# Kernel tuning notes

Hardware: AMD Instinct MI355X
Metric: run time of the kernel (lower is better)

## Reference

```python
import jax, jax.numpy as jnp
import numpy as np

N = 4096          # num_nodes
F = 64            # node_features
H = 128           # hidden_dim
NH = 4            # num_heads
HD = H // NH      # per-head dim = 32
L = 3             # num_layers
C = 7             # num_classes
EDGE_P = 0.004    # ~16 avg degree


def setup_inputs() -> dict:
    key = jax.random.key(0)
    ks = jax.random.split(key, 20)
    g = lambda k, shape, fan_in: jax.random.normal(k, shape, jnp.float32) / np.sqrt(fan_in)
    x = jax.random.normal(ks[0], (N, F), jnp.float32)
    adj = (jax.random.uniform(ks[1], (N, N)) < EDGE_P).astype(jnp.float32)
    return {
        "x": x,
        "adj": adj,
        "enc_W": g(ks[2], (F, H), F), "enc_b": jnp.zeros((H,), jnp.float32),
        "gcn_W": g(ks[3], (L, H, H), H), "gcn_b": jnp.zeros((L, H), jnp.float32),
        "attn_W": g(ks[4], (L, NH, H, HD), H), "attn_Wb": jnp.zeros((L, NH, HD), jnp.float32),
        "attn_a": g(ks[5], (L, NH, 2 * HD), 2 * HD), "attn_ab": jnp.zeros((L, NH), jnp.float32),
        "cls_W1": g(ks[6], (H, H // 2), H), "cls_b1": jnp.zeros((H // 2,), jnp.float32),
        "cls_W2": g(ks[7], (H // 2, C), H // 2), "cls_b2": jnp.zeros((C,), jnp.float32),
        "con_W1": g(ks[8], (H, H // 2), H), "con_b1": jnp.zeros((H // 2,), jnp.float32),
        "con_W2": g(ks[9], (H // 2, 1), H // 2), "con_b2": jnp.zeros((1,), jnp.float32),
    }


def _normalize_adj(adj):
    a = adj + jnp.eye(adj.shape[0], dtype=adj.dtype)
    dinv = jnp.sum(a, axis=1) ** -0.5
    return dinv[:, None] * a * dinv[None, :]


def _gcn(h, adj_norm, W, b):
    support = adj_norm @ h                      # [N,H]
    return jax.nn.relu(support @ W + b)         # dropout=0 (eval)


def _attention(h, edge_mask, W, Wb, a, ab):
    # h:[N,H], W:[NH,H,HD], a:[NH,2*HD]; per-pair score = Linear(concat(h_i,h_j))
    hh = jnp.einsum('nf,hfd->hnd', h, W) + Wb[:, None, :]     # [NH,N,HD]
    a_src, a_dst = a[:, :HD], a[:, HD:]
    s_src = jnp.einsum('hnd,hd->hn', hh, a_src)               # [NH,N]
    s_dst = jnp.einsum('hnd,hd->hn', hh, a_dst)               # [NH,N]
    scores = s_src[:, :, None] + s_dst[:, None, :] + ab[:, None, None]
    # original uses literal 0.0 (NOT -inf) for non-edges before softmax
    scores = jnp.where(edge_mask[None, :, :], scores, 0.0)    # [NH,N,N]
    probs = jax.nn.softmax(scores, axis=-1)
    out = jnp.einsum('hij,hjd->hid', probs, hh)               # [NH,N,HD]
    return out.transpose(1, 0, 2).reshape(h.shape[0], NH * HD)


def reference(x, adj, enc_W, enc_b, gcn_W, gcn_b, attn_W, attn_Wb, attn_a, attn_ab,
              cls_W1, cls_b1, cls_W2, cls_b2, con_W1, con_b1, con_W2, con_b2):
    h = jax.nn.relu(x @ enc_W + enc_b)          # node encoder (dropout=0)
    adj_norm = _normalize_adj(adj)
    edge_mask = adj > 0
    for i in range(L):
        h_gcn = _gcn(h, adj_norm, gcn_W[i], gcn_b[i])
        h_attn = _attention(h, edge_mask, attn_W[i], attn_Wb[i], attn_a[i], attn_ab[i])
        h = jax.nn.relu(h_gcn + h_attn)
    node_logits = jax.nn.relu(h @ cls_W1 + cls_b1) @ cls_W2 + cls_b2
    h_mean = jnp.mean(h, axis=0, keepdims=True)
    contagion = jax.nn.relu(h_mean @ con_W1 + con_b1) @ con_W2 + con_b2
    return (node_logits, h, contagion)
```

## Files before the change

kernel.cpp:

```cpp
#include <hip/hip_runtime.h>

typedef unsigned short u16;
typedef unsigned int u32;

#define N 4096
#define F 64
#define H 128
#define NH 4
#define HD 32
#define EMAX 64

__device__ float g_hA[N * H];
__device__ float g_hB[N * H];
__device__ float g_hhA[N * H];
__device__ float g_hhB[N * H];
__device__ u16   g_cols[N * EMAX];
__device__ int   g_deg[N];
__device__ float g_dinv[N];
__device__ float g_ssrcA[N * NH];
__device__ float g_ssrcB[N * NH];
__device__ float g_sdstA[N * NH];
__device__ float g_sdstB[N * NH];
__device__ float g_part[3][32][H];
__device__ float g_hpart[32][H];

__global__ void k_csr(const float* __restrict__ adj) {
  __shared__ int cnt;
  int row = blockIdx.x;
  if (threadIdx.x == 0) cnt = 0;
  if (row == 0) {
    float* pz = &g_part[0][0][0];
    for (int i = threadIdx.x; i < 3 * 32 * H; i += 256) pz[i] = 0.f;
    float* hz = &g_hpart[0][0];
    for (int i = threadIdx.x; i < 32 * H; i += 256) hz[i] = 0.f;
  }
  __syncthreads();
  int base = threadIdx.x * 16;
  const float4* p = reinterpret_cast<const float4*>(adj + (size_t)row * N + base);
  float4 q0 = p[0], q1 = p[1], q2 = p[2], q3 = p[3];
  float vals[16] = {q0.x, q0.y, q0.z, q0.w, q1.x, q1.y, q1.z, q1.w,
                    q2.x, q2.y, q2.z, q2.w, q3.x, q3.y, q3.z, q3.w};
#pragma unroll
  for (int t = 0; t < 16; ++t)
    if (vals[t] != 0.f) {
      int pos = atomicAdd(&cnt, 1);
      if (pos < EMAX) g_cols[row * EMAX + pos] = (u16)(base + t);
    }
  __syncthreads();
  if (threadIdx.x == 0) {
    g_deg[row] = cnt < EMAX ? cnt : EMAX;
    g_dinv[row] = 1.0f / sqrtf((float)(cnt + 1));
  }
}

__device__ __forceinline__ void agg4(int i0, int tid, const float* __restrict__ h,
                                     const float* __restrict__ hhin,
                                     const float* __restrict__ ssrc_in,
                                     const float* __restrict__ sdst_in,
                                     int l, const float* __restrict__ abv,
                                     int (&jl)[4][EMAX], float (&dv)[4][EMAX],
                                     float (&sdl)[4][EMAX * NH],
                                     float& outa0, float& outa1,
                                     float& sup0, float& sup1) {
  int c = tid & 127, rg = tid >> 7, hc = c >> 5;
  int darr[4];
#pragma unroll
  for (int r = 0; r < 4; ++r) darr[r] = g_deg[i0 + r];
#pragma unroll
  for (int r = 0; r < 4; ++r) {
    const u16* cl = g_cols + (size_t)(i0 + r) * EMAX;
    for (int e = tid; e < darr[r]; e += 256) {
      int j = cl[e];
      jl[r][e] = j;
      dv[r][e] = g_dinv[j];
    }
  }
  __syncthreads();
#pragma unroll
  for (int r = 0; r < 4; ++r)
    for (int idx = tid; idx < darr[r] * NH; idx += 256)
      sdl[r][idx] = sdst_in[jl[r][idx >> 2] * NH + (idx & 3)];
  __syncthreads();

  float sumc = 0.f;
  const float* part = &g_part[l][0][0];
#pragma unroll
  for (int s = 0; s < 32; ++s) sumc += part[s * H + c];
  float ab = abv[hc];

  float oa[2], sp[2];
#pragma unroll
  for (int rr = 0; rr < 2; ++rr) {
    int r = rg * 2 + rr;
    int i = i0 + r, dd = darr[r];
    float ssrc = ssrc_in[i * NH + hc];
    float M = -INFINITY;
    for (int e = 0; e < dd; ++e) M = fmaxf(M, sdl[r][e * NH + hc]);
    float mv = fmaxf(0.f, ssrc + ab + M);
    float em = expf(-mv);
    float base = ssrc + ab - mv;
    float aA = 0.f, aT = 0.f, aG = 0.f, S = 0.f;
    int e = 0;
    for (; e + 2 <= dd; e += 2) {
      int j0 = jl[r][e], j1 = jl[r][e + 1];
      float q0 = hhin[j0 * H + c], q1 = hhin[j1 * H + c];
      float p0 = h[j0 * H + c], p1 = h[j1 * H + c];
      float w0 = expf(base + sdl[r][e * NH + hc]);
      float w1 = expf(base + sdl[r][(e + 1) * NH + hc]);
      aA = fmaf(w0, q0, aA); aA = fmaf(w1, q1, aA);
      aT += q0 + q1;
      aG = fmaf(dv[r][e], p0, aG); aG = fmaf(dv[r][e + 1], p1, aG);
      S += w0 + w1;
    }
    for (; e < dd; ++e) {
      int j = jl[r][e];
      float w = expf(base + sdl[r][e * NH + hc]);
      float q = hhin[j * H + c];
      aA = fmaf(w, q, aA);
      aT += q;
      aG = fmaf(dv[r][e], h[j * H + c], aG);
      S += w;
    }
    float Z = S + em * (float)(N - dd);
    oa[rr] = (aA + em * (sumc - aT)) / Z;
    float di = g_dinv[i];
    sp[rr] = di * (aG + di * h[i * H + c]);
  }
  outa0 = oa[0]; outa1 = oa[1]; sup0 = sp[0]; sup1 = sp[1];
}

__device__ __forceinline__ void proj4(int i0, int tid, const float (&hrowT)[H][4],
                                      const float* __restrict__ aW,
                                      const float* __restrict__ aWb,
                                      const float* __restrict__ aa, int lp,
                                      float* __restrict__ hhout,
                                      float* __restrict__ ssrc_out,
                                      float* __restrict__ sdst_out) {
  int c = tid & 127, rg = tid >> 7, hc = c >> 5, dc = c & 31;
  float b = aWb[hc * HD + dc];
  float p0 = b, p1 = b;
  for (int f = 0; f < H; ++f) {
    float w = aW[(hc * H + f) * HD + dc];
    float2 hv = *reinterpret_cast<const float2*>(&hrowT[f][rg * 2]);
    p0 = fmaf(hv.x, w, p0);
    p1 = fmaf(hv.y, w, p1);
  }
  int r0 = i0 + rg * 2, r1 = r0 + 1;
  hhout[r0 * H + c] = p0;
  hhout[r1 * H + c] = p1;
  const float* ap = aa + hc * 2 * HD;
  float as = ap[dc], ad = ap[HD + dc];
  float ss0 = p0 * as, ss1 = p1 * as, sd0 = p0 * ad, sd1 = p1 * ad;
#pragma unroll
  for (int m = 16; m >= 1; m >>= 1) {
    ss0 += __shfl_xor(ss0, m, 64); ss1 += __shfl_xor(ss1, m, 64);
    sd0 += __shfl_xor(sd0, m, 64); sd1 += __shfl_xor(sd1, m, 64);
  }
  if (dc == 0) {
    ssrc_out[r0 * NH + hc] = ss0; ssrc_out[r1 * NH + hc] = ss1;
    sdst_out[r0 * NH + hc] = sd0; sdst_out[r1 * NH + hc] = sd1;
  }
  atomicAdd(&g_part[lp][r0 & 31][c], p0);
  atomicAdd(&g_part[lp][r1 & 31][c], p1);
}

__global__ void k_enc_proj(const float* __restrict__ x, const float* __restrict__ eW,
                           const float* __restrict__ eb, const float* __restrict__ aW,
                           const float* __restrict__ aWb, const float* __restrict__ aa) {
  __shared__ float xT[F][4];
  __shared__ float hrowT[H][4];
  int i0 = blockIdx.x * 4, tid = threadIdx.x;
  int c = tid & 127, rg = tid >> 7;
  {
    int r = tid >> 6, k = tid & 63;
    xT[k][r] = x[(i0 + r) * F + k];
  }
  __syncthreads();
  float b = eb[c];
  float e0 = b, e1 = b;
  for (int k = 0; k < F; ++k) {
    float w = eW[k * H + c];
    float2 xv = *reinterpret_cast<const float2*>(&xT[k][rg * 2]);
    e0 = fmaf(xv.x, w, e0);
    e1 = fmaf(xv.y, w, e1);
  }
  e0 = fmaxf(e0, 0.f); e1 = fmaxf(e1, 0.f);
  int r0 = i0 + rg * 2, r1 = r0 + 1;
  g_hA[r0 * H + c] = e0; g_hA[r1 * H + c] = e1;
  hrowT[c][rg * 2] = e0; hrowT[c][rg * 2 + 1] = e1;
  __syncthreads();
  proj4(i0, tid, hrowT, aW, aWb, aa, 0, g_hhA, g_ssrcA, g_sdstA);
}

__global__ void k_acp(int pp, int l, const float* __restrict__ gW,
                      const float* __restrict__ gb, const float* __restrict__ aW,
                      const float* __restrict__ aWb, const float* __restrict__ aa,
                      const float* __restrict__ abv) {
  const float* h    = pp ? g_hB : g_hA;
  float*       hout = pp ? g_hA : g_hB;
  const float* hhin = pp ? g_hhB : g_hhA;
  float*       hhout= pp ? g_hhA : g_hhB;
  const float* ssin = pp ? g_ssrcB : g_ssrcA;
  float*       ssout= pp ? g_ssrcA : g_ssrcB;
  const float* sdin = pp ? g_sdstB : g_sdstA;
  float*       sdout= pp ? g_sdstA : g_sdstB;
  __shared__ int   jl[4][EMAX];
  __shared__ float dv[4][EMAX];
  __shared__ float sdl[4][EMAX * NH];
  __shared__ float srowT[H][4];
  __shared__ float hrowT[H][4];
  int i0 = blockIdx.x * 4, tid = threadIdx.x;
  int c = tid & 127, rg = tid >> 7;

  float oa0, oa1, sp0, sp1;
  agg4(i0, tid, h, hhin, ssin, sdin, l, abv, jl, dv, sdl, oa0, oa1, sp0, sp1);
  srowT[c][rg * 2] = sp0; srowT[c][rg * 2 + 1] = sp1;
  __syncthreads();

  float b = gb[c];
  float a0 = b, a1 = b;
  for (int f = 0; f < H; ++f) {
    float w = gW[f * H + c];
    float2 sv = *reinterpret_cast<const float2*>(&srowT[f][rg * 2]);
    a0 = fmaf(sv.x, w, a0);
    a1 = fmaf(sv.y, w, a1);
  }
  float g0 = fmaxf(fmaxf(a0, 0.f) + oa0, 0.f);
  float g1 = fmaxf(fmaxf(a1, 0.f) + oa1, 0.f);
  int r0 = i0 + rg * 2, r1 = r0 + 1;
  hout[r0 * H + c] = g0; hout[r1 * H + c] = g1;
  hrowT[c][rg * 2] = g0; hrowT[c][rg * 2 + 1] = g1;
  __syncthreads();

  proj4(i0, tid, hrowT, aW, aWb, aa, l + 1, hhout, ssout, sdout);
}

__global__ void k_acc(const float* __restrict__ abv, const float* __restrict__ gW,
                      const float* __restrict__ gb,
                      const float* __restrict__ W1, const float* __restrict__ b1,
                      const float* __restrict__ W2, const float* __restrict__ b2,
                      float* __restrict__ out, float* __restrict__ outh) {
  __shared__ int   jl[4][EMAX];
  __shared__ float dv[4][EMAX];
  __shared__ float sdl[4][EMAX * NH];
  __shared__ float srowT[H][4];
  __shared__ float hrowT[H][4];
  __shared__ float tl[4][64];
  int i0 = blockIdx.x * 4, tid = threadIdx.x;
  int c = tid & 127, rg = tid >> 7;

  float oa0, oa1, sp0, sp1;
  agg4(i0, tid, g_hA, g_hhA, g_ssrcA, g_sdstA, 2, abv, jl, dv, sdl, oa0, oa1, sp0, sp1);
  srowT[c][rg * 2] = sp0; srowT[c][rg * 2 + 1] = sp1;
  __syncthreads();

  float b = gb[c];
  float a0 = b, a1 = b;
  for (int f = 0; f < H; ++f) {
    float w = gW[f * H + c];
    float2 sv = *reinterpret_cast<const float2*>(&srowT[f][rg * 2]);
    a0 = fmaf(sv.x, w, a0);
    a1 = fmaf(sv.y, w, a1);
  }
  float g0 = fmaxf(fmaxf(a0, 0.f) + oa0, 0.f);
  float g1 = fmaxf(fmaxf(a1, 0.f) + oa1, 0.f);
  int r0 = i0 + rg * 2, r1 = r0 + 1;
  outh[r0 * H + c] = g0; outh[r1 * H + c] = g1;
  hrowT[c][rg * 2] = g0; hrowT[c][rg * 2 + 1] = g1;
  atomicAdd(&g_hpart[r0 & 31][c], g0);
  atomicAdd(&g_hpart[r1 & 31][c], g1);
  __syncthreads();

  int u = tid & 63, rr4 = tid >> 6;
  float a2 = b1[u];
  for (int f = 0; f < H; ++f) a2 = fmaf(hrowT[f][rr4], W1[f * 64 + u], a2);
  tl[rr4][u] = fmaxf(a2, 0.f);
  __syncthreads();
  if (tid < 28) {
    int r = tid / 7, j = tid - r * 7;
    float p = b2[j];
    for (int v = 0; v < 64; ++v) p = fmaf(tl[r][v], W2[v * 7 + j], p);
    out[(i0 + r) * 7 + j] = p;
  }
}

__global__ void k_contagion(const float* __restrict__ W1, const float* __restrict__ b1,
                            const float* __restrict__ W2, const float* __restrict__ b2,
                            float* __restrict__ out) {
  __shared__ float hm[H];
  __shared__ float tl[64];
  int u = threadIdx.x;
#pragma unroll
  for (int q = 0; q < 2; ++q) {
    int col = u + q * 64;
    float s = 0.f;
#pragma unroll
    for (int sl = 0; sl < 32; ++sl) s += g_hpart[sl][col];
    hm[col] = s * (1.0f / 4096.0f);
  }
  __syncthreads();
  float acc = b1[u];
  for (int f = 0; f < H; ++f) acc = fmaf(hm[f], W1[f * 64 + u], acc);
  tl[u] = fmaxf(acc, 0.f);
  __syncthreads();
  if (u == 0) {
    float p = b2[0];
    for (int v = 0; v < 64; ++v) p = fmaf(tl[v], W2[v], p);
    out[0] = p;
  }
}

extern "C" void kernel_launch(void* const* d_in, const int* in_sizes, int n_in,
                              void* d_out, int out_size, void* d_ws, size_t ws_size,
                              hipStream_t stream) {
  const float* x       = (const float*)d_in[0];
  const float* adj     = (const float*)d_in[1];
  const float* enc_W   = (const float*)d_in[2];
  const float* enc_b   = (const float*)d_in[3];
  const float* gcn_W   = (const float*)d_in[4];
  const float* gcn_b   = (const float*)d_in[5];
  const float* attn_W  = (const float*)d_in[6];
  const float* attn_Wb = (const float*)d_in[7];
  const float* attn_a  = (const float*)d_in[8];
  const float* attn_ab = (const float*)d_in[9];
  const float* cls_W1  = (const float*)d_in[10];
  const float* cls_b1  = (const float*)d_in[11];
  const float* cls_W2  = (const float*)d_in[12];
  const float* cls_b2  = (const float*)d_in[13];
  const float* con_W1  = (const float*)d_in[14];
  const float* con_b1  = (const float*)d_in[15];
  const float* con_W2  = (const float*)d_in[16];
  const float* con_b2  = (const float*)d_in[17];
  (void)in_sizes; (void)n_in; (void)d_ws; (void)ws_size; (void)out_size;

  float* out = (float*)d_out;
  float* outh = out + (size_t)N * 7;
  float* outc = out + (size_t)N * 7 + (size_t)N * H;

  k_csr<<<N, 256, 0, stream>>>(adj);
  k_enc_proj<<<N / 4, 256, 0, stream>>>(x, enc_W, enc_b, attn_W, attn_Wb, attn_a);
  k_acp<<<N / 4, 256, 0, stream>>>(0, 0, gcn_W, gcn_b,
                                   attn_W + (size_t)1 * NH * H * HD,
                                   attn_Wb + (size_t)1 * NH * HD,
                                   attn_a + (size_t)1 * NH * 2 * HD, attn_ab);
  k_acp<<<N / 4, 256, 0, stream>>>(1, 1, gcn_W + (size_t)1 * H * H, gcn_b + H,
                                   attn_W + (size_t)2 * NH * H * HD,
                                   attn_Wb + (size_t)2 * NH * HD,
                                   attn_a + (size_t)2 * NH * 2 * HD, attn_ab + NH);
  k_acc<<<N / 4, 256, 0, stream>>>(attn_ab + 2 * NH, gcn_W + (size_t)2 * H * H,
                                   gcn_b + 2 * H, cls_W1, cls_b1, cls_W2, cls_b2,
                                   out, outh);
  k_contagion<<<1, 64, 0, stream>>>(con_W1, con_b1, con_W2, con_b2, outc);
}
```

Measured before the change: 230.4 us.

## Fuse CSR construction into encoder/projection kernel and move buffer zeroing to end

```diff
diff --git a/kernel.cpp b/kernel.cpp
--- a/kernel.cpp
+++ b/kernel.cpp
@@ -23,35 +23,6 @@
 __device__ float g_sdstB[N * NH];
 __device__ float g_part[3][32][H];
 __device__ float g_hpart[32][H];
-
-__global__ void k_csr(const float* __restrict__ adj) {
-  __shared__ int cnt;
-  int row = blockIdx.x;
-  if (threadIdx.x == 0) cnt = 0;
-  if (row == 0) {
-    float* pz = &g_part[0][0][0];
-    for (int i = threadIdx.x; i < 3 * 32 * H; i += 256) pz[i] = 0.f;
-    float* hz = &g_hpart[0][0];
-    for (int i = threadIdx.x; i < 32 * H; i += 256) hz[i] = 0.f;
-  }
-  __syncthreads();
-  int base = threadIdx.x * 16;
-  const float4* p = reinterpret_cast<const float4*>(adj + (size_t)row * N + base);
-  float4 q0 = p[0], q1 = p[1], q2 = p[2], q3 = p[3];
-  float vals[16] = {q0.x, q0.y, q0.z, q0.w, q1.x, q1.y, q1.z, q1.w,
-                    q2.x, q2.y, q2.z, q2.w, q3.x, q3.y, q3.z, q3.w};
-#pragma unroll
-  for (int t = 0; t < 16; ++t)
-    if (vals[t] != 0.f) {
-      int pos = atomicAdd(&cnt, 1);
-      if (pos < EMAX) g_cols[row * EMAX + pos] = (u16)(base + t);
-    }
-  __syncthreads();
-  if (threadIdx.x == 0) {
-    g_deg[row] = cnt < EMAX ? cnt : EMAX;
-    g_dinv[row] = 1.0f / sqrtf((float)(cnt + 1));
-  }
-}
 
 __device__ __forceinline__ void agg4(int i0, int tid, const float* __restrict__ h,
                                      const float* __restrict__ hhin,
@@ -164,18 +135,40 @@
   atomicAdd(&g_part[lp][r1 & 31][c], p1);
 }
 
-__global__ void k_enc_proj(const float* __restrict__ x, const float* __restrict__ eW,
-                           const float* __restrict__ eb, const float* __restrict__ aW,
-                           const float* __restrict__ aWb, const float* __restrict__ aa) {
+__global__ void k_prep(const float* __restrict__ adj, const float* __restrict__ x,
+                       const float* __restrict__ eW, const float* __restrict__ eb,
+                       const float* __restrict__ aW, const float* __restrict__ aWb,
+                       const float* __restrict__ aa) {
   __shared__ float xT[F][4];
   __shared__ float hrowT[H][4];
+  __shared__ int   cnt4[4];
   int i0 = blockIdx.x * 4, tid = threadIdx.x;
   int c = tid & 127, rg = tid >> 7;
+
+  if (tid < 4) cnt4[tid] = 0;
+  __syncthreads();
   {
-    int r = tid >> 6, k = tid & 63;
-    xT[k][r] = x[(i0 + r) * F + k];
-  }
-  __syncthreads();
+    int r = tid >> 6, u = tid & 63;
+    int row = i0 + r;
+    const float4* p = reinterpret_cast<const float4*>(adj + (size_t)row * N) + u;
+#pragma unroll
+    for (int k = 0; k < 16; ++k) {
+      float4 v = p[k * 64];
+      int base = (u + k * 64) * 4;
+      if (v.x != 0.f) { int q = atomicAdd(&cnt4[r], 1); if (q < EMAX) g_cols[row * EMAX + q] = (u16)(base); }
+      if (v.y != 0.f) { int q = atomicAdd(&cnt4[r], 1); if (q < EMAX) g_cols[row * EMAX + q] = (u16)(base + 1); }
+      if (v.z != 0.f) { int q = atomicAdd(&cnt4[r], 1); if (q < EMAX) g_cols[row * EMAX + q] = (u16)(base + 2); }
+      if (v.w != 0.f) { int q = atomicAdd(&cnt4[r], 1); if (q < EMAX) g_cols[row * EMAX + q] = (u16)(base + 3); }
+    }
+    xT[tid & 63][tid >> 6] = x[(i0 + (tid >> 6)) * F + (tid & 63)];
+  }
+  __syncthreads();
+  if (tid < 4) {
+    int cnt = cnt4[tid];
+    g_deg[i0 + tid] = cnt < EMAX ? cnt : EMAX;
+    g_dinv[i0 + tid] = 1.0f / sqrtf((float)(cnt + 1));
+  }
+
   float b = eb[c];
   float e0 = b, e1 = b;
   for (int k = 0; k < F; ++k) {
@@ -289,25 +282,29 @@
                             float* __restrict__ out) {
   __shared__ float hm[H];
   __shared__ float tl[64];
-  int u = threadIdx.x;
-#pragma unroll
-  for (int q = 0; q < 2; ++q) {
-    int col = u + q * 64;
+  int tid = threadIdx.x;
+  {
     float s = 0.f;
 #pragma unroll
-    for (int sl = 0; sl < 32; ++sl) s += g_hpart[sl][col];
-    hm[col] = s * (1.0f / 4096.0f);
-  }
-  __syncthreads();
-  float acc = b1[u];
-  for (int f = 0; f < H; ++f) acc = fmaf(hm[f], W1[f * 64 + u], acc);
-  tl[u] = fmaxf(acc, 0.f);
-  __syncthreads();
-  if (u == 0) {
+    for (int sl = 0; sl < 32; ++sl) s += g_hpart[sl][tid];
+    hm[tid] = s * (1.0f / 4096.0f);
+  }
+  __syncthreads();
+  if (tid < 64) {
+    float acc = b1[tid];
+    for (int f = 0; f < H; ++f) acc = fmaf(hm[f], W1[f * 64 + tid], acc);
+    tl[tid] = fmaxf(acc, 0.f);
+  }
+  __syncthreads();
+  if (tid == 0) {
     float p = b2[0];
     for (int v = 0; v < 64; ++v) p = fmaf(tl[v], W2[v], p);
     out[0] = p;
   }
+  float* pz = &g_part[0][0][0];
+  for (int i = tid; i < 3 * 32 * H; i += 128) pz[i] = 0.f;
+  float* hz = &g_hpart[0][0];
+  for (int i = tid; i < 32 * H; i += 128) hz[i] = 0.f;
 }
 
 extern "C" void kernel_launch(void* const* d_in, const int* in_sizes, int n_in,
@@ -337,8 +334,7 @@
   float* outh = out + (size_t)N * 7;
   float* outc = out + (size_t)N * 7 + (size_t)N * H;
 
-  k_csr<<<N, 256, 0, stream>>>(adj);
-  k_enc_proj<<<N / 4, 256, 0, stream>>>(x, enc_W, enc_b, attn_W, attn_Wb, attn_a);
+  k_prep<<<N / 4, 256, 0, stream>>>(adj, x, enc_W, enc_b, attn_W, attn_Wb, attn_a);
   k_acp<<<N / 4, 256, 0, stream>>>(0, 0, gcn_W, gcn_b,
                                    attn_W + (size_t)1 * NH * H * HD,
                                    attn_Wb + (size_t)1 * NH * HD,
@@ -350,5 +346,5 @@
   k_acc<<<N / 4, 256, 0, stream>>>(attn_ab + 2 * NH, gcn_W + (size_t)2 * H * H,
                                    gcn_b + 2 * H, cls_W1, cls_b1, cls_W2, cls_b2,
                                    out, outh);
-  k_contagion<<<1, 64, 0, stream>>>(con_W1, con_b1, con_W2, con_b2, outc);
-}
+  k_contagion<<<1, 128, 0, stream>>>(con_W1, con_b1, con_W2, con_b2, outc);
+}
```

Result: no change. 232.6 us (+1.0%).
